# Optimization experiments

Measured on AMD Instinct MI355X. Metric: run time of the kernel, lower is better.

The kernel has to match this reference:

```python
import jax, jax.numpy as jnp
import numpy as np

N_NODES = 100000
N_EDGES = 1600000
F_IN = 128
HIDDEN = 128
N_CLASSES = 2
N_GRAPHS = 512


def setup_inputs() -> dict:
    key = jax.random.key(0)
    ks = jax.random.split(key, 10)
    node_features = jax.random.normal(ks[0], (N_NODES, F_IN), dtype=jnp.float32)
    edge_index = jax.random.randint(ks[1], (2, N_EDGES), 0, N_NODES, dtype=jnp.int64)
    batch = jnp.sort(jax.random.randint(ks[2], (N_NODES,), 0, N_GRAPHS, dtype=jnp.int64))
    s1 = 1.0 / np.sqrt(F_IN)
    s2 = 1.0 / np.sqrt(HIDDEN)
    W1 = jax.random.uniform(ks[3], (F_IN, HIDDEN), jnp.float32, -s1, s1)
    b1 = jnp.zeros((HIDDEN,), jnp.float32)
    W2 = jax.random.uniform(ks[4], (HIDDEN, HIDDEN), jnp.float32, -s2, s2)
    b2 = jnp.zeros((HIDDEN,), jnp.float32)
    Wlin = jax.random.uniform(ks[5], (HIDDEN, N_CLASSES), jnp.float32, -s2, s2)
    blin = jax.random.uniform(ks[6], (N_CLASSES,), jnp.float32, -s2, s2)
    return {"node_features": node_features, "edge_index": edge_index, "batch": batch,
            "W1": W1, "b1": b1, "W2": W2, "b2": b2, "Wlin": Wlin, "blin": blin}


def _gcn_conv(x, src, dst, norm, W, b, n_nodes):
    # transform-then-propagate (PyG GCNConv default)
    h = x @ W                                   # [N, H]
    msg = h[src] * norm[:, None]                # gather + edge scale
    out = jax.ops.segment_sum(msg, dst, num_segments=n_nodes)  # scatter-add
    return out + b


def reference(node_features, edge_index, batch, W1, b1, W2, b2, Wlin, blin):
    n = node_features.shape[0]
    loop = jnp.arange(n, dtype=edge_index.dtype)
    src = jnp.concatenate([edge_index[0], loop])  # add self-loops
    dst = jnp.concatenate([edge_index[1], loop])
    # symmetric degree normalization: deg counts incoming edges incl. self-loop
    deg = jax.ops.segment_sum(jnp.ones_like(src, dtype=node_features.dtype), dst, num_segments=n)
    dis = jnp.where(deg > 0, jax.lax.rsqrt(jnp.maximum(deg, 1.0)), 0.0)
    norm = dis[src] * dis[dst]

    x = jax.nn.relu(_gcn_conv(node_features, src, dst, norm, W1, b1, n))
    x = jax.nn.relu(_gcn_conv(x, src, dst, norm, W2, b2, n))

    # global mean pool over graphs
    ones = jnp.ones((n,), dtype=x.dtype)
    counts = jax.ops.segment_sum(ones, batch, num_segments=N_GRAPHS)
    sums = jax.ops.segment_sum(x, batch, num_segments=N_GRAPHS)
    pooled = sums / jnp.maximum(counts, 1.0)[:, None]

    # dropout is identity in eval mode
    return pooled @ Wlin + blin
```

## Files before the change

kernel.cpp:

```cpp
#include <hip/hip_runtime.h>
#include <hip/hip_bf16.h>
#include <hip/hip_fp16.h>

constexpr int NN = 100000;
constexpr int NE = 1600000;
constexpr int NG = 512;
constexpr int F  = 128;

constexpr int NB   = 392;
constexpr int RCAP = 4608;
constexpr int CAP  = 32;
constexpr int NCH  = 8;
constexpr int BINB = 512;

typedef _Float16 f16;
typedef f16 f16x2 __attribute__((ext_vector_type(2)));
typedef f16 f16x4 __attribute__((ext_vector_type(4)));
typedef f16 f16x8 __attribute__((ext_vector_type(8)));
typedef float f32x4 __attribute__((ext_vector_type(4)));
typedef unsigned int u32;
typedef u32 u32x4a __attribute__((ext_vector_type(4), aligned(4)));

__global__ void prep_w(const float* __restrict__ W1, const float* __restrict__ W2,
                       f16* __restrict__ WT1, f16* __restrict__ WT2,
                       int* __restrict__ gcur) {
    int idx = blockIdx.x * blockDim.x + threadIdx.x;
    if (idx < NB) gcur[idx] = idx * RCAP;
    if (idx < 128 * 128) {
        int n = idx >> 7, k = idx & 127;
        WT1[idx] = (f16)W1[k * 128 + n];
        WT2[idx] = (f16)W2[k * 128 + n];
    }
}

__global__ __launch_bounds__(256) void bin_edges(const int* __restrict__ ei,
                                                 int* __restrict__ gcur,
                                                 u32* __restrict__ binned) {
    __shared__ u32 stage[NB][CAP];
    __shared__ int scnt[NB];
    for (int b = threadIdx.x; b < NB; b += 256) scnt[b] = 0;
    __syncthreads();
    const int per = NE / BINB;
    const int e0 = blockIdx.x * per;
    for (int r = 0; r < per; r += 256) {
        int k = r + threadIdx.x;
        if (k < per) {
            int e = e0 + k;
            int s = __builtin_nontemporal_load(&ei[e]);
            int d = __builtin_nontemporal_load(&ei[NE + e]);
            int b = d >> 8;
            u32 v = ((u32)(d & 255) << 24) | (u32)s;
            int p = atomicAdd(&scnt[b], 1);
            if (p < CAP) stage[b][p] = v;
        }
        __syncthreads();
        for (int b2 = threadIdx.x; b2 < NB; b2 += 256) {
            int n = scnt[b2];
            if (n >= 16) {
                int f = n & ~15;
                int base = atomicAdd(&gcur[b2], f);
                const u32x4a* st4 = (const u32x4a*)&stage[b2][0];
                u32x4a* out4 = (u32x4a*)&binned[base];
                for (int j = 0; j < (f >> 2); j++) out4[j] = st4[j];
                for (int j = 0; j < n - f; j++) stage[b2][j] = stage[b2][f + j];
                scnt[b2] = n - f;
            }
        }
        __syncthreads();
    }
    for (int b2 = threadIdx.x; b2 < NB; b2 += 256) {
        int n = scnt[b2];
        if (n > 0) {
            int base = atomicAdd(&gcur[b2], n);
            for (int j = 0; j < n; j++) binned[base + j] = stage[b2][j];
        }
    }
}

__global__ void scan_buckets(const int* __restrict__ gcur, int* __restrict__ bucketBase,
                             int* __restrict__ offs) {
    __shared__ int tmp[512];
    int t = threadIdx.x;
    int c = (t < NB) ? (gcur[t] - t * RCAP) : 0;
    tmp[t] = c;
    __syncthreads();
    for (int d = 1; d < 512; d <<= 1) {
        int x = (t >= d) ? tmp[t - d] : 0;
        __syncthreads();
        tmp[t] += x;
        __syncthreads();
    }
    if (t < NB) bucketBase[t] = tmp[t] - c;
    if (t == 0) offs[NN] = NE;
}

__global__ __launch_bounds__(256) void build_csr(const u32* __restrict__ binned,
                                                 const int* __restrict__ gcur,
                                                 const int* __restrict__ bucketBase,
                                                 int* __restrict__ offs,
                                                 float* __restrict__ dis,
                                                 int* __restrict__ csr_src) {
    __shared__ u32 ed[RCAP];
    __shared__ u32 lcsr[RCAP];
    __shared__ int hist[256];
    __shared__ int loff[256];
    __shared__ int lcur[256];
    const int b = blockIdx.x;
    int cnt = gcur[b] - b * RCAP;
    if (cnt > RCAP) cnt = RCAP;
    const int gbase = bucketBase[b];
    const int t = threadIdx.x;
    hist[t] = 0;
    __syncthreads();
    for (int j = t; j < cnt; j += 256) {
        u32 v = __builtin_nontemporal_load(&binned[(size_t)b * RCAP + j]);
        ed[j] = v;
        atomicAdd(&hist[v >> 24], 1);
    }
    __syncthreads();
    int h = hist[t];
    loff[t] = h;
    __syncthreads();
    for (int d = 1; d < 256; d <<= 1) {
        int x = (t >= d) ? loff[t - d] : 0;
        __syncthreads();
        loff[t] += x;
        __syncthreads();
    }
    int excl = loff[t] - h;
    lcur[t] = excl;
    int node = (b << 8) + t;
    if (node < NN) {
        offs[node] = gbase + excl;
        dis[node] = rsqrtf((float)(h + 1));
    }
    __syncthreads();
    for (int j = t; j < cnt; j += 256) {
        u32 v = ed[j];
        int p = atomicAdd(&lcur[v >> 24], 1);
        lcsr[p] = v & 0x1FFFFu;
    }
    __syncthreads();
    for (int j = t; j < cnt; j += 256) csr_src[gbase + j] = (int)lcsr[j];
}

template<bool IN_HALF>
__global__ __launch_bounds__(256) void gemm_direct(const void* __restrict__ Xv,
                                                   const f16* __restrict__ WT,
                                                   const float* __restrict__ dis,
                                                   f16* __restrict__ H, int M) {
    const int tid = threadIdx.x;
    const int wid = tid >> 6;
    const int lane = tid & 63;
    const int row0 = blockIdx.x * 128;
    const int wrow = wid * 32;
    const int lr = lane & 15;
    const int lk = (lane >> 4) * 8;
    f32x4 acc[2][8] = {};
    #pragma unroll
    for (int ks = 0; ks < 4; ks++) {
        f16x8 a[2], b[8];
        #pragma unroll
        for (int mf = 0; mf < 2; mf++) {
            int row = row0 + wrow + mf * 16 + lr;
            row = row < M ? row : M - 1;
            if (IN_HALF) {
                a[mf] = *(const f16x8*)((const f16*)Xv + (size_t)row * 128 + ks * 32 + lk);
            } else {
                const float* Xf = (const float*)Xv + (size_t)row * 128 + ks * 32 + lk;
                float4 v0 = *(const float4*)Xf;
                float4 v1 = *(const float4*)(Xf + 4);
                a[mf] = f16x8{(f16)v0.x, (f16)v0.y, (f16)v0.z, (f16)v0.w,
                              (f16)v1.x, (f16)v1.y, (f16)v1.z, (f16)v1.w};
            }
        }
        #pragma unroll
        for (int nf = 0; nf < 8; nf++)
            b[nf] = *(const f16x8*)(WT + (size_t)(nf * 16 + lr) * 128 + ks * 32 + lk);
        #pragma unroll
        for (int mf = 0; mf < 2; mf++)
            #pragma unroll
            for (int nf = 0; nf < 8; nf++)
                acc[mf][nf] = __builtin_amdgcn_mfma_f32_16x16x32_f16(a[mf], b[nf], acc[mf][nf], 0, 0, 0);
    }
    const int crow = (lane >> 4) * 4;
    #pragma unroll
    for (int mf = 0; mf < 2; mf++) {
        #pragma unroll
        for (int reg = 0; reg < 4; reg++) {
            int row = row0 + wrow + mf * 16 + crow + reg;
            if (row < M) {
                float sc = dis[row];
                #pragma unroll
                for (int nf = 0; nf < 8; nf++)
                    H[(size_t)row * 128 + nf * 16 + lr] = (f16)(acc[mf][nf][reg] * sc);
            }
        }
    }
}

__device__ __forceinline__ void gather_rows(const f16* __restrict__ h, int i,
                                            const int* __restrict__ offs,
                                            const int* __restrict__ csr_src,
                                            int q, int r, float acc[8]) {
    if (q == 0) {
        f16x8 v = *(const f16x8*)(h + (size_t)i * F + r * 8);
        #pragma unroll
        for (int j = 0; j < 8; j++) acc[j] = (float)v[j];
    }
    const int s = offs[i], e = offs[i + 1];
    int t = s + q;
    for (; t + 12 < e; t += 16) {
        int sr0 = __builtin_nontemporal_load(&csr_src[t]);
        int sr1 = __builtin_nontemporal_load(&csr_src[t + 4]);
        int sr2 = __builtin_nontemporal_load(&csr_src[t + 8]);
        int sr3 = __builtin_nontemporal_load(&csr_src[t + 12]);
        f16x8 v0 = *(const f16x8*)(h + (size_t)sr0 * F + r * 8);
        f16x8 v1 = *(const f16x8*)(h + (size_t)sr1 * F + r * 8);
        f16x8 v2 = *(const f16x8*)(h + (size_t)sr2 * F + r * 8);
        f16x8 v3 = *(const f16x8*)(h + (size_t)sr3 * F + r * 8);
        #pragma unroll
        for (int j = 0; j < 8; j++)
            acc[j] += ((float)v0[j] + (float)v1[j]) + ((float)v2[j] + (float)v3[j]);
    }
    for (; t < e; t += 4) {
        int sr = __builtin_nontemporal_load(&csr_src[t]);
        f16x8 v = *(const f16x8*)(h + (size_t)sr * F + r * 8);
        #pragma unroll
        for (int j = 0; j < 8; j++) acc[j] += (float)v[j];
    }
    #pragma unroll
    for (int j = 0; j < 8; j++) {
        acc[j] += __shfl_xor(acc[j], 16);
        acc[j] += __shfl_xor(acc[j], 32);
    }
}

__global__ __launch_bounds__(256) void aggregate16(const f16* __restrict__ h,
                                                   const int* __restrict__ offs,
                                                   const int* __restrict__ csr_src,
                                                   const float* __restrict__ dis,
                                                   const float* __restrict__ bias,
                                                   f16* __restrict__ out, int n) {
    int i = blockIdx.x * 4 + (threadIdx.x >> 6);
    if (i >= n) return;
    const int lane = threadIdx.x & 63;
    const int q = lane >> 4;
    const int r = lane & 15;
    float acc[8] = {};
    gather_rows(h, i, offs, csr_src, q, r, acc);
    if (q == 0) {
        float di = dis[i];
        const float4* b4 = (const float4*)bias;
        float4 bb0 = b4[r * 2], bb1 = b4[r * 2 + 1];
        float bb[8] = {bb0.x, bb0.y, bb0.z, bb0.w, bb1.x, bb1.y, bb1.z, bb1.w};
        f16x8 o;
        #pragma unroll
        for (int j = 0; j < 8; j++) {
            float v = fmaf(acc[j], di, bb[j]);
            o[j] = (f16)(v > 0.f ? v : 0.f);
        }
        *(f16x8*)(out + (size_t)i * F + r * 8) = o;
    }
}

__global__ __launch_bounds__(256) void pool_partial(const f16* __restrict__ x,
                                                    const int* __restrict__ batch,
                                                    float* __restrict__ partial, int n) {
    int g = blockIdx.x;
    __shared__ int se[2];
    if (threadIdx.x < 2) {
        int target = g + threadIdx.x;
        int lo = 0, hi = n;
        while (lo < hi) {
            int mid = (lo + hi) >> 1;
            if (batch[mid] < target) lo = mid + 1; else hi = mid;
        }
        se[threadIdx.x] = lo;
    }
    __syncthreads();
    int s = se[0], e = se[1];
    int wid = threadIdx.x >> 6, lane = threadIdx.x & 63;
    int slot = blockIdx.y * 4 + wid;
    float a0 = 0.f, a1 = 0.f;
    const f16x2* x2 = (const f16x2*)x;
    for (int i = s + slot; i < e; i += 4 * NCH) {
        f16x2 v = x2[(size_t)i * 64 + lane];
        a0 += (float)v[0];
        a1 += (float)v[1];
    }
    __shared__ float red[4][128];
    red[wid][lane * 2] = a0;
    red[wid][lane * 2 + 1] = a1;
    __syncthreads();
    if (wid == 0) {
        float s0 = red[0][lane * 2] + red[1][lane * 2] + red[2][lane * 2] + red[3][lane * 2];
        float s1 = red[0][lane * 2 + 1] + red[1][lane * 2 + 1] + red[2][lane * 2 + 1] + red[3][lane * 2 + 1];
        float2* pp = (float2*)&partial[((size_t)g * NCH + blockIdx.y) * F];
        pp[lane] = make_float2(s0, s1);
    }
}

__global__ __launch_bounds__(128) void pool_final(const float* __restrict__ partial,
                                                  const int* __restrict__ batch,
                                                  const float* __restrict__ Wlin,
                                                  const float* __restrict__ blin,
                                                  float* __restrict__ out, int n) {
    int g = blockIdx.x;
    int f = threadIdx.x;
    __shared__ int se[2];
    if (threadIdx.x < 2) {
        int target = g + threadIdx.x;
        int lo = 0, hi = n;
        while (lo < hi) {
            int mid = (lo + hi) >> 1;
            if (batch[mid] < target) lo = mid + 1; else hi = mid;
        }
        se[threadIdx.x] = lo;
    }
    __syncthreads();
    int s = se[0], e = se[1];
    float acc = 0.f;
    #pragma unroll
    for (int c = 0; c < NCH; c++) acc += partial[((size_t)g * NCH + c) * F + f];
    float cnt = (float)((e - s) > 0 ? (e - s) : 1);
    float p = acc / cnt;
    float v0 = p * Wlin[f * 2 + 0];
    float v1 = p * Wlin[f * 2 + 1];
    #pragma unroll
    for (int o = 32; o > 0; o >>= 1) {
        v0 += __shfl_xor(v0, o);
        v1 += __shfl_xor(v1, o);
    }
    __shared__ float red[4];
    int wid = threadIdx.x >> 6;
    if ((threadIdx.x & 63) == 0) { red[wid * 2] = v0; red[wid * 2 + 1] = v1; }
    __syncthreads();
    if (threadIdx.x == 0) {
        out[g * 2 + 0] = red[0] + red[2] + blin[0];
        out[g * 2 + 1] = red[1] + red[3] + blin[1];
    }
}

extern "C" void kernel_launch(void* const* d_in, const int* in_sizes, int n_in,
                              void* d_out, int out_size, void* d_ws, size_t ws_size,
                              hipStream_t stream) {
    const float* X     = (const float*)d_in[0];
    const int*   ei    = (const int*)d_in[1];
    const int*   batch = (const int*)d_in[2];
    const float* W1    = (const float*)d_in[3];
    const float* b1    = (const float*)d_in[4];
    const float* W2    = (const float*)d_in[5];
    const float* b2    = (const float*)d_in[6];
    const float* Wlin  = (const float*)d_in[7];
    const float* blin  = (const float*)d_in[8];
    float* out = (float*)d_out;

    char* p = (char*)d_ws;
    auto alloc = [&](size_t bytes) -> char* {
        char* r = p;
        p += (bytes + 255) & ~size_t(255);
        return r;
    };
    int*   gcur       = (int*)alloc((size_t)NB * 4);
    int*   bucketBase = (int*)alloc((size_t)NB * 4);
    int*   offs       = (int*)alloc((size_t)(NN + 1) * 4);
    float* dis        = (float*)alloc((size_t)NN * 4);
    u32*   binned     = (u32*)alloc((size_t)NB * RCAP * 4);
    int*   csr_src    = (int*)alloc((size_t)NE * 4);
    f16*   WT1        = (f16*)alloc((size_t)128 * 128 * 2);
    f16*   WT2        = (f16*)alloc((size_t)128 * 128 * 2);
    f16*   bufA       = (f16*)alloc((size_t)NN * F * 2);
    f16*   bufB       = (f16*)alloc((size_t)NN * F * 2);
    float* partial    = (float*)alloc((size_t)NG * NCH * F * 4);

    prep_w<<<64, 256, 0, stream>>>(W1, W2, WT1, WT2, gcur);
    bin_edges<<<BINB, 256, 0, stream>>>(ei, gcur, binned);
    scan_buckets<<<1, 512, 0, stream>>>(gcur, bucketBase, offs);
    build_csr<<<NB, 256, 0, stream>>>(binned, gcur, bucketBase, offs, dis, csr_src);

    gemm_direct<false><<<(NN + 127) / 128, 256, 0, stream>>>(X, WT1, dis, bufA, NN);
    aggregate16<<<(NN + 3) / 4, 256, 0, stream>>>(bufA, offs, csr_src, dis, b1, bufB, NN);
    gemm_direct<true><<<(NN + 127) / 128, 256, 0, stream>>>(bufB, WT2, dis, bufA, NN);
    aggregate16<<<(NN + 3) / 4, 256, 0, stream>>>(bufA, offs, csr_src, dis, b2, bufB, NN);
    pool_partial<<<dim3(NG, NCH), 256, 0, stream>>>(bufB, batch, partial, NN);
    pool_final<<<NG, 128, 0, stream>>>(partial, batch, Wlin, blin, out, NN);
}
```

Measured before the change: 273.1 us.

## Fuse CSR build with layer-1 GEMM and move source scaling into aggregation

The layer-1 GEMM no longer depends on the degree normalisation, so it runs inside the same launch as CSR construction (extra blocks beyond the bucket blocks), with an all-ones scale. The source-side normalisation is instead applied per gathered neighbour in a new layer-1 aggregation, at the cost of an extra dis[] lookup per edge. Weight prep is merged into the binning kernel, gcur is zeroed by memset and stored as a relative count, and the gather unroll drops from 4 to 2 with the nontemporal index loads removed. This aims to cut launches and let the GEMM overlap the CSR build, but adds random reads to the layer-1 gather.

Measured after the change: 262.7 us. -3.8%, faster.

```diff
diff --git a/kernel.cpp b/kernel.cpp
--- a/kernel.cpp
+++ b/kernel.cpp
@@ -12,6 +12,7 @@
 constexpr int CAP  = 32;
 constexpr int NCH  = 8;
 constexpr int BINB = 512;
+constexpr int GEMB = (NN + 127) / 128;
 
 typedef _Float16 f16;
 typedef f16 f16x2 __attribute__((ext_vector_type(2)));
@@ -21,23 +22,77 @@
 typedef unsigned int u32;
 typedef u32 u32x4a __attribute__((ext_vector_type(4), aligned(4)));
 
-__global__ void prep_w(const float* __restrict__ W1, const float* __restrict__ W2,
-                       f16* __restrict__ WT1, f16* __restrict__ WT2,
-                       int* __restrict__ gcur) {
-    int idx = blockIdx.x * blockDim.x + threadIdx.x;
-    if (idx < NB) gcur[idx] = idx * RCAP;
-    if (idx < 128 * 128) {
+template<bool IN_HALF>
+__device__ __forceinline__ void gemm_body(int bid, int tid,
+                                          const void* __restrict__ Xv,
+                                          const f16* __restrict__ WT,
+                                          const float* __restrict__ dis,
+                                          f16* __restrict__ H, int M) {
+    const int wid = tid >> 6;
+    const int lane = tid & 63;
+    const int row0 = bid * 128;
+    const int wrow = wid * 32;
+    const int lr = lane & 15;
+    const int lk = (lane >> 4) * 8;
+    f32x4 acc[2][8] = {};
+    #pragma unroll
+    for (int ks = 0; ks < 4; ks++) {
+        f16x8 a[2], b[8];
+        #pragma unroll
+        for (int mf = 0; mf < 2; mf++) {
+            int row = row0 + wrow + mf * 16 + lr;
+            row = row < M ? row : M - 1;
+            if (IN_HALF) {
+                a[mf] = *(const f16x8*)((const f16*)Xv + (size_t)row * 128 + ks * 32 + lk);
+            } else {
+                const float* Xf = (const float*)Xv + (size_t)row * 128 + ks * 32 + lk;
+                float4 v0 = *(const float4*)Xf;
+                float4 v1 = *(const float4*)(Xf + 4);
+                a[mf] = f16x8{(f16)v0.x, (f16)v0.y, (f16)v0.z, (f16)v0.w,
+                              (f16)v1.x, (f16)v1.y, (f16)v1.z, (f16)v1.w};
+            }
+        }
+        #pragma unroll
+        for (int nf = 0; nf < 8; nf++)
+            b[nf] = *(const f16x8*)(WT + (size_t)(nf * 16 + lr) * 128 + ks * 32 + lk);
+        #pragma unroll
+        for (int mf = 0; mf < 2; mf++)
+            #pragma unroll
+            for (int nf = 0; nf < 8; nf++)
+                acc[mf][nf] = __builtin_amdgcn_mfma_f32_16x16x32_f16(a[mf], b[nf], acc[mf][nf], 0, 0, 0);
+    }
+    const int crow = (lane >> 4) * 4;
+    #pragma unroll
+    for (int mf = 0; mf < 2; mf++) {
+        #pragma unroll
+        for (int reg = 0; reg < 4; reg++) {
+            int row = row0 + wrow + mf * 16 + crow + reg;
+            if (row < M) {
+                float sc = dis[row];
+                #pragma unroll
+                for (int nf = 0; nf < 8; nf++)
+                    H[(size_t)row * 128 + nf * 16 + lr] = (f16)(acc[mf][nf][reg] * sc);
+            }
+        }
+    }
+}
+
+__global__ __launch_bounds__(256) void k1_bin_prepw(const int* __restrict__ ei,
+                                                    int* __restrict__ gcur,
+                                                    u32* __restrict__ binned,
+                                                    const float* __restrict__ W1,
+                                                    const float* __restrict__ W2,
+                                                    f16* __restrict__ WT1,
+                                                    f16* __restrict__ WT2) {
+    __shared__ u32 stage[NB][CAP];
+    __shared__ int scnt[NB];
+    if (blockIdx.x >= BINB) {
+        int idx = (blockIdx.x - BINB) * 256 + threadIdx.x;
         int n = idx >> 7, k = idx & 127;
         WT1[idx] = (f16)W1[k * 128 + n];
         WT2[idx] = (f16)W2[k * 128 + n];
-    }
-}
-
-__global__ __launch_bounds__(256) void bin_edges(const int* __restrict__ ei,
-                                                 int* __restrict__ gcur,
-                                                 u32* __restrict__ binned) {
-    __shared__ u32 stage[NB][CAP];
-    __shared__ int scnt[NB];
+        return;
+    }
     for (int b = threadIdx.x; b < NB; b += 256) scnt[b] = 0;
     __syncthreads();
     const int per = NE / BINB;
@@ -58,7 +113,7 @@
             int n = scnt[b2];
             if (n >= 16) {
                 int f = n & ~15;
-                int base = atomicAdd(&gcur[b2], f);
+                int base = b2 * RCAP + atomicAdd(&gcur[b2], f);
                 const u32x4a* st4 = (const u32x4a*)&stage[b2][0];
                 u32x4a* out4 = (u32x4a*)&binned[base];
                 for (int j = 0; j < (f >> 2); j++) out4[j] = st4[j];
@@ -71,7 +126,7 @@
     for (int b2 = threadIdx.x; b2 < NB; b2 += 256) {
         int n = scnt[b2];
         if (n > 0) {
-            int base = atomicAdd(&gcur[b2], n);
+            int base = b2 * RCAP + atomicAdd(&gcur[b2], n);
             for (int j = 0; j < n; j++) binned[base + j] = stage[b2][j];
         }
     }
@@ -81,7 +136,7 @@
                              int* __restrict__ offs) {
     __shared__ int tmp[512];
     int t = threadIdx.x;
-    int c = (t < NB) ? (gcur[t] - t * RCAP) : 0;
+    int c = (t < NB) ? gcur[t] : 0;
     tmp[t] = c;
     __syncthreads();
     for (int d = 1; d < 512; d <<= 1) {
@@ -94,19 +149,27 @@
     if (t == 0) offs[NN] = NE;
 }
 
-__global__ __launch_bounds__(256) void build_csr(const u32* __restrict__ binned,
-                                                 const int* __restrict__ gcur,
-                                                 const int* __restrict__ bucketBase,
-                                                 int* __restrict__ offs,
-                                                 float* __restrict__ dis,
-                                                 int* __restrict__ csr_src) {
+__global__ __launch_bounds__(256) void k3_csr_gemm1(const u32* __restrict__ binned,
+                                                    const int* __restrict__ gcur,
+                                                    const int* __restrict__ bucketBase,
+                                                    int* __restrict__ offs,
+                                                    float* __restrict__ dis,
+                                                    int* __restrict__ csr_src,
+                                                    const float* __restrict__ X,
+                                                    const f16* __restrict__ WT1,
+                                                    const float* __restrict__ degdis,
+                                                    f16* __restrict__ H) {
     __shared__ u32 ed[RCAP];
     __shared__ u32 lcsr[RCAP];
     __shared__ int hist[256];
     __shared__ int loff[256];
     __shared__ int lcur[256];
+    if (blockIdx.x >= NB) {
+        gemm_body<false>(blockIdx.x - NB, threadIdx.x, X, WT1, degdis, H, NN);
+        return;
+    }
     const int b = blockIdx.x;
-    int cnt = gcur[b] - b * RCAP;
+    int cnt = gcur[b];
     if (cnt > RCAP) cnt = RCAP;
     const int gbase = bucketBase[b];
     const int t = threadIdx.x;
@@ -144,58 +207,41 @@
     for (int j = t; j < cnt; j += 256) csr_src[gbase + j] = (int)lcsr[j];
 }
 
-template<bool IN_HALF>
-__global__ __launch_bounds__(256) void gemm_direct(const void* __restrict__ Xv,
-                                                   const f16* __restrict__ WT,
+
+__device__ __forceinline__ void gather_rows_scaled(const f16* __restrict__ h, int i,
+                                                   const int* __restrict__ offs,
+                                                   const int* __restrict__ csr_src,
                                                    const float* __restrict__ dis,
-                                                   f16* __restrict__ H, int M) {
-    const int tid = threadIdx.x;
-    const int wid = tid >> 6;
-    const int lane = tid & 63;
-    const int row0 = blockIdx.x * 128;
-    const int wrow = wid * 32;
-    const int lr = lane & 15;
-    const int lk = (lane >> 4) * 8;
-    f32x4 acc[2][8] = {};
-    #pragma unroll
-    for (int ks = 0; ks < 4; ks++) {
-        f16x8 a[2], b[8];
-        #pragma unroll
-        for (int mf = 0; mf < 2; mf++) {
-            int row = row0 + wrow + mf * 16 + lr;
-            row = row < M ? row : M - 1;
-            if (IN_HALF) {
-                a[mf] = *(const f16x8*)((const f16*)Xv + (size_t)row * 128 + ks * 32 + lk);
-            } else {
-                const float* Xf = (const float*)Xv + (size_t)row * 128 + ks * 32 + lk;
-                float4 v0 = *(const float4*)Xf;
-                float4 v1 = *(const float4*)(Xf + 4);
-                a[mf] = f16x8{(f16)v0.x, (f16)v0.y, (f16)v0.z, (f16)v0.w,
-                              (f16)v1.x, (f16)v1.y, (f16)v1.z, (f16)v1.w};
-            }
-        }
-        #pragma unroll
-        for (int nf = 0; nf < 8; nf++)
-            b[nf] = *(const f16x8*)(WT + (size_t)(nf * 16 + lr) * 128 + ks * 32 + lk);
-        #pragma unroll
-        for (int mf = 0; mf < 2; mf++)
-            #pragma unroll
-            for (int nf = 0; nf < 8; nf++)
-                acc[mf][nf] = __builtin_amdgcn_mfma_f32_16x16x32_f16(a[mf], b[nf], acc[mf][nf], 0, 0, 0);
-    }
-    const int crow = (lane >> 4) * 4;
-    #pragma unroll
-    for (int mf = 0; mf < 2; mf++) {
-        #pragma unroll
-        for (int reg = 0; reg < 4; reg++) {
-            int row = row0 + wrow + mf * 16 + crow + reg;
-            if (row < M) {
-                float sc = dis[row];
-                #pragma unroll
-                for (int nf = 0; nf < 8; nf++)
-                    H[(size_t)row * 128 + nf * 16 + lr] = (f16)(acc[mf][nf][reg] * sc);
-            }
-        }
+                                                   int q, int r, float acc[8]) {
+    if (q == 0) {
+        f16x8 v = *(const f16x8*)(h + (size_t)i * F + r * 8);
+        float di = dis[i];
+        #pragma unroll
+        for (int j = 0; j < 8; j++) acc[j] = (float)v[j] * di;
+    }
+    const int s = offs[i], e = offs[i + 1];
+    int t = s + q;
+    for (; t + 4 < e; t += 8) {
+        int sr0 = csr_src[t];
+        int sr1 = csr_src[t + 4];
+        float d0 = dis[sr0], d1 = dis[sr1];
+        f16x8 v0 = *(const f16x8*)(h + (size_t)sr0 * F + r * 8);
+        f16x8 v1 = *(const f16x8*)(h + (size_t)sr1 * F + r * 8);
+        #pragma unroll
+        for (int j = 0; j < 8; j++)
+            acc[j] += (float)v0[j] * d0 + (float)v1[j] * d1;
+    }
+    if (t < e) {
+        int sr = csr_src[t];
+        float d0 = dis[sr];
+        f16x8 v = *(const f16x8*)(h + (size_t)sr * F + r * 8);
+        #pragma unroll
+        for (int j = 0; j < 8; j++) acc[j] += (float)v[j] * d0;
+    }
+    #pragma unroll
+    for (int j = 0; j < 8; j++) {
+        acc[j] += __shfl_xor(acc[j], 16);
+        acc[j] += __shfl_xor(acc[j], 32);
     }
 }
 
@@ -210,21 +256,16 @@
     }
     const int s = offs[i], e = offs[i + 1];
     int t = s + q;
-    for (; t + 12 < e; t += 16) {
-        int sr0 = __builtin_nontemporal_load(&csr_src[t]);
-        int sr1 = __builtin_nontemporal_load(&csr_src[t + 4]);
-        int sr2 = __builtin_nontemporal_load(&csr_src[t + 8]);
-        int sr3 = __builtin_nontemporal_load(&csr_src[t + 12]);
+    for (; t + 4 < e; t += 8) {
+        int sr0 = csr_src[t];
+        int sr1 = csr_src[t + 4];
         f16x8 v0 = *(const f16x8*)(h + (size_t)sr0 * F + r * 8);
         f16x8 v1 = *(const f16x8*)(h + (size_t)sr1 * F + r * 8);
-        f16x8 v2 = *(const f16x8*)(h + (size_t)sr2 * F + r * 8);
-        f16x8 v3 = *(const f16x8*)(h + (size_t)sr3 * F + r * 8);
-        #pragma unroll
-        for (int j = 0; j < 8; j++)
-            acc[j] += ((float)v0[j] + (float)v1[j]) + ((float)v2[j] + (float)v3[j]);
-    }
-    for (; t < e; t += 4) {
-        int sr = __builtin_nontemporal_load(&csr_src[t]);
+        #pragma unroll
+        for (int j = 0; j < 8; j++) acc[j] += (float)v0[j] + (float)v1[j];
+    }
+    if (t < e) {
+        int sr = csr_src[t];
         f16x8 v = *(const f16x8*)(h + (size_t)sr * F + r * 8);
         #pragma unroll
         for (int j = 0; j < 8; j++) acc[j] += (float)v[j];
@@ -236,12 +277,40 @@
     }
 }
 
-__global__ __launch_bounds__(256) void aggregate16(const f16* __restrict__ h,
-                                                   const int* __restrict__ offs,
-                                                   const int* __restrict__ csr_src,
-                                                   const float* __restrict__ dis,
-                                                   const float* __restrict__ bias,
-                                                   f16* __restrict__ out, int n) {
+__global__ __launch_bounds__(256) void aggregate_l1(const f16* __restrict__ h,
+                                                    const int* __restrict__ offs,
+                                                    const int* __restrict__ csr_src,
+                                                    const float* __restrict__ dis,
+                                                    const float* __restrict__ bias,
+                                                    f16* __restrict__ out, int n) {
+    int i = blockIdx.x * 4 + (threadIdx.x >> 6);
+    if (i >= n) return;
+    const int lane = threadIdx.x & 63;
+    const int q = lane >> 4;
+    const int r = lane & 15;
+    float acc[8] = {};
+    gather_rows_scaled(h, i, offs, csr_src, dis, q, r, acc);
+    if (q == 0) {
+        float di = dis[i];
+        const float4* b4 = (const float4*)bias;
+        float4 bb0 = b4[r * 2], bb1 = b4[r * 2 + 1];
+        float bb[8] = {bb0.x, bb0.y, bb0.z, bb0.w, bb1.x, bb1.y, bb1.z, bb1.w};
+        f16x8 o;
+        #pragma unroll
+        for (int j = 0; j < 8; j++) {
+            float v = fmaf(acc[j], di, bb[j]);
+            o[j] = (f16)(v > 0.f ? v : 0.f);
+        }
+        *(f16x8*)(out + (size_t)i * F + r * 8) = o;
+    }
+}
+
+__global__ __launch_bounds__(256) void aggregate_l2(const f16* __restrict__ h,
+                                                    const int* __restrict__ offs,
+                                                    const int* __restrict__ csr_src,
+                                                    const float* __restrict__ dis,
+                                                    const float* __restrict__ bias,
+                                                    f16* __restrict__ out, int n) {
     int i = blockIdx.x * 4 + (threadIdx.x >> 6);
     if (i >= n) return;
     const int lane = threadIdx.x & 63;
@@ -262,6 +331,13 @@
         }
         *(f16x8*)(out + (size_t)i * F + r * 8) = o;
     }
+}
+
+__global__ __launch_bounds__(256) void gemm2(const f16* __restrict__ Xh,
+                                             const f16* __restrict__ WT,
+                                             const float* __restrict__ dis,
+                                             f16* __restrict__ H, int M) {
+    gemm_body<true>(blockIdx.x, threadIdx.x, Xh, WT, dis, H, M);
 }
 
 __global__ __launch_bounds__(256) void pool_partial(const f16* __restrict__ x,
@@ -373,16 +449,25 @@
     f16*   bufA       = (f16*)alloc((size_t)NN * F * 2);
     f16*   bufB       = (f16*)alloc((size_t)NN * F * 2);
     float* partial    = (float*)alloc((size_t)NG * NCH * F * 4);
-
-    prep_w<<<64, 256, 0, stream>>>(W1, W2, WT1, WT2, gcur);
-    bin_edges<<<BINB, 256, 0, stream>>>(ei, gcur, binned);
+    float* ones       = (float*)alloc((size_t)NN * 4);
+
+    hipMemsetAsync(gcur, 0, (size_t)NB * 4, stream);
+    extern __global__ void fill_ones(float*, int);
+    fill_ones<<<(NN + 255) / 256, 256, 0, stream>>>(ones, NN);
+
+    k1_bin_prepw<<<BINB + 64, 256, 0, stream>>>(ei, gcur, binned, W1, W2, WT1, WT2);
     scan_buckets<<<1, 512, 0, stream>>>(gcur, bucketBase, offs);
-    build_csr<<<NB, 256, 0, stream>>>(binned, gcur, bucketBase, offs, dis, csr_src);
-
-    gemm_direct<false><<<(NN + 127) / 128, 256, 0, stream>>>(X, WT1, dis, bufA, NN);
-    aggregate16<<<(NN + 3) / 4, 256, 0, stream>>>(bufA, offs, csr_src, dis, b1, bufB, NN);
-    gemm_direct<true><<<(NN + 127) / 128, 256, 0, stream>>>(bufB, WT2, dis, bufA, NN);
-    aggregate16<<<(NN + 3) / 4, 256, 0, stream>>>(bufA, offs, csr_src, dis, b2, bufB, NN);
+    k3_csr_gemm1<<<NB + GEMB, 256, 0, stream>>>(binned, gcur, bucketBase, offs, dis,
+                                                csr_src, X, WT1, ones, bufA);
+
+    aggregate_l1<<<(NN + 3) / 4, 256, 0, stream>>>(bufA, offs, csr_src, dis, b1, bufB, NN);
+    gemm2<<<GEMB, 256, 0, stream>>>(bufB, WT2, dis, bufA, NN);
+    aggregate_l2<<<(NN + 3) / 4, 256, 0, stream>>>(bufA, offs, csr_src, dis, b2, bufB, NN);
     pool_partial<<<dim3(NG, NCH), 256, 0, stream>>>(bufB, batch, partial, NN);
     pool_final<<<NG, 128, 0, stream>>>(partial, batch, Wlin, blin, out, NN);
 }
+
+__global__ void fill_ones(float* __restrict__ v, int n) {
+    int i = blockIdx.x * blockDim.x + threadIdx.x;
+    if (i < n) v[i] = 1.0f;
+}
```
